# Kernel tuning notes

Measured on AMD Instinct MI355X. Metric: run time of the kernel, lower is better.

Reference implementation:

```python
import jax, jax.numpy as jnp
import numpy as np

B = 1024
NUM_DENSE = 13
NUM_SPARSE = 26
VOCAB = 100000
EMB_DIM = 16
BOT = [512, 256, 64, 16]
TOP = [1024, 512, 256]
D_INT = BOT[-1] + NUM_SPARSE * EMB_DIM  # 432
OUT_INT = D_INT * (D_INT + 1) // 2      # 93528


def setup_inputs() -> dict:
    key = jax.random.key(0)
    ks = jax.random.split(key, 32)
    inp = {
        "dense_features": jax.random.normal(ks[0], (B, NUM_DENSE), jnp.float32),
        "sparse_features": jax.random.randint(ks[1], (B, NUM_SPARSE), 0, VOCAB),
        "emb_tables": jax.random.normal(ks[2], (NUM_SPARSE, VOCAB, EMB_DIM), jnp.float32) * 0.02,
    }
    # bottom MLP weights (in, out) convention
    dims = [NUM_DENSE] + BOT
    for i in range(len(BOT)):
        inp[f"bw{i}"] = jax.random.normal(ks[3 + i], (dims[i], dims[i + 1]), jnp.float32) * 0.02
        inp[f"bb{i}"] = jnp.zeros((dims[i + 1],), jnp.float32)
    tdims = [BOT[-1] + OUT_INT] + TOP + [1]
    for i in range(len(TOP) + 1):
        inp[f"tw{i}"] = jax.random.normal(ks[10 + i], (tdims[i], tdims[i + 1]), jnp.float32) * 0.02
        inp[f"tb{i}"] = jnp.zeros((tdims[i + 1],), jnp.float32)
    return inp


def _forward(dense_features, emb_tables, bws, bbs, tws, tbs, sparse_features):
    # bottom MLP: Linear+ReLU stacks
    h = dense_features
    for w, b in zip(bws, bbs):
        h = jax.nn.relu(h @ w + b)
    dense_out = h  # (B, 16)
    # embedding lookups: table t indexed by column t of sparse_features
    # emb_tables: (F, V, E); gather per-table then flatten -> (B, F*E)
    emb = jnp.take_along_axis(
        emb_tables[None],  # (1, F, V, E)
        sparse_features.T[None, :, :, None].transpose(0, 1, 2, 3) * 0 + sparse_features.T[None, :, :, None],
        axis=2,
    )  # placeholder avoided below
    # cleaner: vmap over tables
    emb = jax.vmap(lambda tbl, idx: tbl[idx], in_axes=(0, 1))(emb_tables, sparse_features)  # (F, B, E)
    emb = jnp.transpose(emb, (1, 0, 2)).reshape(dense_features.shape[0], -1)  # (B, F*E)
    x = jnp.concatenate([dense_out, emb], axis=1)  # (B, D_INT)
    # pairwise interaction: upper triangle (incl. diagonal) of outer product.
    iu0, iu1 = np.triu_indices(x.shape[1])
    inter = x[:, iu0] * x[:, iu1]  # (B, OUT_INT) -- only needed entries
    z = jnp.concatenate([dense_out, inter], axis=1)
    n_top = len(tws)
    for i, (w, b) in enumerate(zip(tws, tbs)):
        z = z @ w + b
        if i < n_top - 1:
            z = jax.nn.relu(z)
    return z


def reference(dense_features, sparse_features, emb_tables,
              bw0, bb0, bw1, bb1, bw2, bb2, bw3, bb3,
              tw0, tb0, tw1, tb1, tw2, tb2, tw3, tb3):
    bws = [bw0, bw1, bw2, bw3]
    bbs = [bb0, bb1, bb2, bb3]
    tws = [tw0, tw1, tw2, tw3]
    tbs = [tb0, tb1, tb2, tb3]
    return _forward(dense_features, emb_tables, bws, bbs, tws, tbs, sparse_features)
```

## Files before the change

### kernel.cpp

```cpp
#include <hip/hip_runtime.h>
#include <stdint.h>

typedef unsigned short ushort_t;
typedef __attribute__((ext_vector_type(4))) float f32x4;
typedef __attribute__((ext_vector_type(8))) short s16x8;

#define DEVFN static __device__ __forceinline__

constexpr int B_   = 1024;
constexpr int P_   = 93528;
constexpr int K1   = 93544;
constexpr int Kp   = 94208;
constexpr int SPLITS = 16;
constexpr int KCH  = Kp / SPLITS;
constexpr int KSTEPS = KCH / 64;

DEVFN ushort_t f2bf(float f) {
  union { float f; unsigned int u; } x; x.f = f;
  unsigned int r = x.u + 0x7FFFu + ((x.u >> 16) & 1u);
  return (ushort_t)(r >> 16);
}

DEVFN void gload_lds16(const void* g, void* l) {
  __builtin_amdgcn_global_load_lds((const __attribute__((address_space(1))) unsigned int*)g,
                                   (__attribute__((address_space(3))) unsigned int*)l, 16, 0, 0);
}

__global__ __launch_bounds__(256) void k_iu(int* __restrict__ iu, float* __restrict__ xT) {
  int k = blockIdx.x * 256 + threadIdx.x;
  if (blockIdx.x < 8) {
    int idx = blockIdx.x * 256 + threadIdx.x;
    xT[432 * 1024 + idx] = (idx < 1024) ? 1.f : 0.f;
  }
  if (k >= Kp) return;
  int v;
  if (k < 16) v = k | (432 << 16);
  else if (k >= K1) v = 433 | (433 << 16);
  else {
    int p = k - 16;
    float s = sqrtf((float)(748225 - 8 * p));
    int i = (int)((865.0f - s) * 0.5f);
    if (i < 0) i = 0; if (i > 431) i = 431;
    while (i < 431 && (i + 1) * (865 - (i + 1)) / 2 <= p) ++i;
    while (i > 0 && i * (865 - i) / 2 > p) --i;
    int j = i + (p - i * (865 - i) / 2);
    v = i | (j << 16);
  }
  iu[k] = v;
}

__global__ __launch_bounds__(256) void k_bot(const float* __restrict__ dense,
    const float* __restrict__ bw0, const float* __restrict__ bb0,
    const float* __restrict__ bw1, const float* __restrict__ bb1,
    const float* __restrict__ bw2, const float* __restrict__ bb2,
    const float* __restrict__ bw3, const float* __restrict__ bb3,
    float* __restrict__ xT) {
  __shared__ float xs[16 * 13];
  __shared__ float h1[16 * 512];
  __shared__ float h2[16 * 256];
  __shared__ float h3[16 * 64];
  int t = threadIdx.x, m0 = blockIdx.x * 16;
  if (t < 208) xs[t] = dense[m0 * 13 + t];
  __syncthreads();
  #pragma unroll
  for (int h = 0; h < 2; ++h) {
    int n = h * 256 + t;
    float a[16];
    float bv = bb0[n];
    #pragma unroll
    for (int r = 0; r < 16; ++r) a[r] = bv;
    for (int k = 0; k < 13; ++k) {
      float w = bw0[k * 512 + n];
      #pragma unroll
      for (int r = 0; r < 16; ++r) a[r] = fmaf(xs[r * 13 + k], w, a[r]);
    }
    #pragma unroll
    for (int r = 0; r < 16; ++r) h1[r * 512 + n] = fmaxf(a[r], 0.f);
  }
  __syncthreads();
  {
    int n = t;
    float a[16];
    float bv = bb1[n];
    #pragma unroll
    for (int r = 0; r < 16; ++r) a[r] = bv;
    for (int k = 0; k < 512; ++k) {
      float w = bw1[k * 256 + n];
      #pragma unroll
      for (int r = 0; r < 16; ++r) a[r] = fmaf(h1[r * 512 + k], w, a[r]);
    }
    #pragma unroll
    for (int r = 0; r < 16; ++r) h2[r * 256 + n] = fmaxf(a[r], 0.f);
  }
  __syncthreads();
  {
    int n = t & 63, r0 = t >> 6;
    float a[4];
    float bv = bb2[n];
    #pragma unroll
    for (int i = 0; i < 4; ++i) a[i] = bv;
    for (int k = 0; k < 256; ++k) {
      float w = bw2[k * 64 + n];
      #pragma unroll
      for (int i = 0; i < 4; ++i) a[i] = fmaf(h2[(r0 + 4 * i) * 256 + k], w, a[i]);
    }
    #pragma unroll
    for (int i = 0; i < 4; ++i) h3[(r0 + 4 * i) * 64 + n] = fmaxf(a[i], 0.f);
  }
  __syncthreads();
  {
    int n = t & 15, r = t >> 4;
    float a = bb3[n];
    for (int k = 0; k < 64; ++k) a = fmaf(h3[r * 64 + k], bw3[k * 16 + n], a);
    xT[(size_t)n * B_ + m0 + r] = fmaxf(a, 0.f);
  }
}

template<int K, int N>
__global__ __launch_bounds__(256) void k_sgemm(const float* __restrict__ A,
                                               const float* __restrict__ W,
                                               const float* __restrict__ bias,
                                               float* __restrict__ C) {
  __shared__ float As[16][34];
  __shared__ float Bs[16][68];
  int t = threadIdx.x;
  int m0 = blockIdx.x * 32, n0 = blockIdx.y * 64;
  int tx = t & 15, ty = t >> 4;
  float acc[2][4];
  #pragma unroll
  for (int j = 0; j < 2; ++j)
    #pragma unroll
    for (int q = 0; q < 4; ++q) acc[j][q] = 0.f;
  int ar = t >> 3, ak = (t & 7) * 2;
  int bk = t >> 4, bn = (t & 15) * 4;
  for (int k0 = 0; k0 < K; k0 += 16) {
    float2 av = *(const float2*)&A[(size_t)(m0 + ar) * K + k0 + ak];
    float4 bv = *(const float4*)&W[(size_t)(k0 + bk) * N + n0 + bn];
    __syncthreads();
    As[ak][ar] = av.x; As[ak + 1][ar] = av.y;
    *(float4*)&Bs[bk][bn] = bv;
    __syncthreads();
    #pragma unroll
    for (int k = 0; k < 16; ++k) {
      float2 a = *(const float2*)&As[k][ty * 2];
      float4 b = *(const float4*)&Bs[k][tx * 4];
      acc[0][0] = fmaf(a.x, b.x, acc[0][0]); acc[0][1] = fmaf(a.x, b.y, acc[0][1]);
      acc[0][2] = fmaf(a.x, b.z, acc[0][2]); acc[0][3] = fmaf(a.x, b.w, acc[0][3]);
      acc[1][0] = fmaf(a.y, b.x, acc[1][0]); acc[1][1] = fmaf(a.y, b.y, acc[1][1]);
      acc[1][2] = fmaf(a.y, b.z, acc[1][2]); acc[1][3] = fmaf(a.y, b.w, acc[1][3]);
    }
  }
  #pragma unroll
  for (int j = 0; j < 2; ++j) {
    int m = m0 + ty * 2 + j;
    float4 o;
    o.x = fmaxf(acc[j][0] + bias[n0 + tx * 4 + 0], 0.f);
    o.y = fmaxf(acc[j][1] + bias[n0 + tx * 4 + 1], 0.f);
    o.z = fmaxf(acc[j][2] + bias[n0 + tx * 4 + 2], 0.f);
    o.w = fmaxf(acc[j][3] + bias[n0 + tx * 4 + 3], 0.f);
    *(float4*)&C[(size_t)m * N + n0 + tx * 4] = o;
  }
}

__global__ __launch_bounds__(256) void k_emb(const int* __restrict__ sparse,
                                             const float* __restrict__ tbl,
                                             float* __restrict__ xT) {
  int f = blockIdx.x;
  int b = blockIdx.y * 256 + threadIdx.x;
  int idx = sparse[(size_t)b * 26 + f];
  const float4* src = (const float4*)(tbl + ((size_t)f * 100000 + idx) * 16);
  #pragma unroll
  for (int q = 0; q < 4; ++q) {
    float4 v = src[q];
    int r = 16 + f * 16 + q * 4;
    xT[(size_t)(r + 0) * B_ + b] = v.x;
    xT[(size_t)(r + 1) * B_ + b] = v.y;
    xT[(size_t)(r + 2) * B_ + b] = v.z;
    xT[(size_t)(r + 3) * B_ + b] = v.w;
  }
}

__global__ __launch_bounds__(256, 4) void k_genz(const float* __restrict__ xT,
                                                 const int* __restrict__ iu,
                                                 ushort_t* __restrict__ Z) {
  __shared__ int ls_iu[512];
  int t = threadIdx.x, l = t & 63, w = t >> 6;
  int mb = blockIdx.x * 64;
  int kt = blockIdx.y * 512;
  ls_iu[t] = iu[kt + t];
  ls_iu[256 + t] = iu[kt + 256 + t];
  __syncthreads();
  uint32_t moff = mb + l;
  int kw = w * 128;
  #pragma unroll 2
  for (int g = 0; g < 16; ++g) {
    int kloc = kw + g * 8;
    int4 ij0 = *(const int4*)&ls_iu[kloc];
    int4 ij1 = *(const int4*)&ls_iu[kloc + 4];
    float p[8];
    {
      int v0 = ij0.x, v1 = ij0.y, v2 = ij0.z, v3 = ij0.w;
      p[0] = xT[(uint32_t)((v0 & 0xFFFF) << 10) + moff] * xT[(uint32_t)((v0 >> 16) << 10) + moff];
      p[1] = xT[(uint32_t)((v1 & 0xFFFF) << 10) + moff] * xT[(uint32_t)((v1 >> 16) << 10) + moff];
      p[2] = xT[(uint32_t)((v2 & 0xFFFF) << 10) + moff] * xT[(uint32_t)((v2 >> 16) << 10) + moff];
      p[3] = xT[(uint32_t)((v3 & 0xFFFF) << 10) + moff] * xT[(uint32_t)((v3 >> 16) << 10) + moff];
      v0 = ij1.x; v1 = ij1.y; v2 = ij1.z; v3 = ij1.w;
      p[4] = xT[(uint32_t)((v0 & 0xFFFF) << 10) + moff] * xT[(uint32_t)((v0 >> 16) << 10) + moff];
      p[5] = xT[(uint32_t)((v1 & 0xFFFF) << 10) + moff] * xT[(uint32_t)((v1 >> 16) << 10) + moff];
      p[6] = xT[(uint32_t)((v2 & 0xFFFF) << 10) + moff] * xT[(uint32_t)((v2 >> 16) << 10) + moff];
      p[7] = xT[(uint32_t)((v3 & 0xFFFF) << 10) + moff] * xT[(uint32_t)((v3 >> 16) << 10) + moff];
    }
    union { uint32_t w[4]; int4 v4; } o;
    asm("v_cvt_pk_bf16_f32 %0, %1, %2" : "=v"(o.w[0]) : "v"(p[0]), "v"(p[1]));
    asm("v_cvt_pk_bf16_f32 %0, %1, %2" : "=v"(o.w[1]) : "v"(p[2]), "v"(p[3]));
    asm("v_cvt_pk_bf16_f32 %0, %1, %2" : "=v"(o.w[2]) : "v"(p[4]), "v"(p[5]));
    asm("v_cvt_pk_bf16_f32 %0, %1, %2" : "=v"(o.w[3]) : "v"(p[6]), "v"(p[7]));
    int kglob = kt + kloc;
    *(int4*)&Z[((size_t)(kglob >> 3) * 1024 + moff) * 8] = o.v4;
  }
}

__global__ __launch_bounds__(256) void k_wt(const float* __restrict__ tw0,
                                            ushort_t* __restrict__ WT) {
  __shared__ ushort_t ls[256 * 68];
  int t = threadIdx.x;
  int k0 = blockIdx.x * 256, n0 = blockIdx.y * 64;
  int kr = t >> 2, c4 = t & 3;
  #pragma unroll
  for (int pass = 0; pass < 4; ++pass) {
    int kl = pass * 64 + kr;
    int k = k0 + kl;
    #pragma unroll
    for (int q = 0; q < 4; ++q) {
      float4 v = make_float4(0.f, 0.f, 0.f, 0.f);
      if (k < K1) v = *(const float4*)&tw0[(size_t)k * 1024 + n0 + q * 16 + c4 * 4];
      ushort_t* d = &ls[kl * 68 + q * 16 + c4 * 4];
      d[0] = f2bf(v.x); d[1] = f2bf(v.y); d[2] = f2bf(v.z); d[3] = f2bf(v.w);
    }
  }
  __syncthreads();
  int nl = t >> 2, kq = t & 3;
  ushort_t* dst = WT + (size_t)(n0 + nl) * Kp + k0 + kq * 64;
  #pragma unroll
  for (int j = 0; j < 8; ++j) {
    union { ushort_t u[8]; int4 v; } o;
    #pragma unroll
    for (int e = 0; e < 8; ++e) o.u[e] = ls[(kq * 64 + j * 8 + e) * 68 + nl];
    *(int4*)(dst + j * 8) = o.v;
  }
}

__global__ __launch_bounds__(512, 2) void k_gemm(const ushort_t* __restrict__ Z,
                                                 const ushort_t* __restrict__ WT,
                                                 float* __restrict__ part) {
  __shared__ ushort_t lds[65536];
  int t = threadIdx.x;
  int bid = blockIdx.x;
  int s = bid >> 4, tile = bid & 15;
  int m0 = (tile >> 2) * 256, n0 = (tile & 3) * 256;
  int kb = s * KCH;

  int rr = t >> 3, cc = t & 7;
  int cs = cc ^ (rr & 7);
  const ushort_t* pa0 = Z + (((size_t)(kb >> 3) + cs) * 1024 + m0 + rr) * 8;
  const ushort_t* pb0 = WT + (size_t)(n0 + rr) * Kp + kb + cs * 8;
  const size_t rowStrideB = (size_t)64 * Kp;
  int l0 = t * 8;

  int w = t >> 6, l = t & 63;
  int wm = (w >> 2) * 128, wn = (w & 3) * 64;
  int lhi = l >> 4, llo = l & 15;

  f32x4 acc[8][4];
  #pragma unroll
  for (int a = 0; a < 8; ++a)
    #pragma unroll
    for (int b = 0; b < 4; ++b) acc[a][b] = f32x4{0.f, 0.f, 0.f, 0.f};

  #pragma unroll
  for (int i = 0; i < 4; ++i)
    gload_lds16(pb0 + i * rowStrideB, &lds[32768 + i * 4096 + l0]);
  gload_lds16(pa0,            &lds[0 * 4096 + l0]);
  gload_lds16(pa0 + 2 * 512,  &lds[2 * 4096 + l0]);
  gload_lds16(pa0 + 1 * 512,  &lds[1 * 4096 + l0]);
  gload_lds16(pa0 + 3 * 512,  &lds[3 * 4096 + l0]);

  for (int tt = 0; tt < KSTEPS; ++tt) {
    const ushort_t* Ab = &lds[(tt & 1) * 16384];
    const ushort_t* Bb = &lds[32768 + (tt & 1) * 16384];
    bool pf = (tt + 1 < KSTEPS);
    ushort_t* dA = &lds[((tt + 1) & 1) * 16384];
    ushort_t* dB = &lds[32768 + ((tt + 1) & 1) * 16384];
    const ushort_t* sA = pa0 + (size_t)(tt + 1) * 65536;
    const ushort_t* sB = pb0 + (size_t)(tt + 1) * 64;
    s16x8 bf[4][2];

    asm volatile("s_waitcnt vmcnt(2)" ::: "memory");
    __builtin_amdgcn_s_barrier();
    __builtin_amdgcn_sched_barrier(0);
    if (pf) {
      gload_lds16(sB,              dB + l0);
      gload_lds16(sB + rowStrideB, dB + 4096 + l0);
    }
    #pragma unroll
    for (int nf = 0; nf < 4; ++nf)
      #pragma unroll
      for (int ks = 0; ks < 2; ++ks) {
        int row = wn + nf * 16 + llo;
        int ch = (ks * 4 + lhi) ^ (row & 7);
        bf[nf][ks] = *(const s16x8*)&Bb[row * 64 + ch * 8];
      }
    #pragma unroll
    for (int q = 0; q < 4; ++q) {
      if (q == 1 && pf) {
        gload_lds16(sB + 2 * rowStrideB, dB + 2 * 4096 + l0);
        gload_lds16(sB + 3 * rowStrideB, dB + 3 * 4096 + l0);
      }
      if (q == 2) {
        if (pf) asm volatile("s_waitcnt vmcnt(4)" ::: "memory");
        else    asm volatile("s_waitcnt vmcnt(0)" ::: "memory");
        __builtin_amdgcn_s_barrier();
        __builtin_amdgcn_sched_barrier(0);
        if (pf) {
          gload_lds16(sA,           dA + l0);
          gload_lds16(sA + 2 * 512, dA + 2 * 4096 + l0);
        }
      }
      if (q == 3 && pf) {
        gload_lds16(sA + 1 * 512, dA + 1 * 4096 + l0);
        gload_lds16(sA + 3 * 512, dA + 3 * 4096 + l0);
      }
      s16x8 af[2][2];
      #pragma unroll
      for (int j = 0; j < 2; ++j)
        #pragma unroll
        for (int ks = 0; ks < 2; ++ks) {
          int row = wm + (q * 2 + j) * 16 + llo;
          int ch = (ks * 4 + lhi) ^ (row & 7);
          af[j][ks] = *(const s16x8*)&Ab[row * 64 + ch * 8];
        }
      __builtin_amdgcn_s_setprio(1);
      #pragma unroll
      for (int j = 0; j < 2; ++j)
        #pragma unroll
        for (int nf = 0; nf < 4; ++nf)
          #pragma unroll
          for (int ks = 0; ks < 2; ++ks)
            acc[q * 2 + j][nf] = __builtin_amdgcn_mfma_f32_16x16x32_bf16(af[j][ks], bf[nf][ks], acc[q * 2 + j][nf], 0, 0, 0);
      __builtin_amdgcn_s_setprio(0);
    }
  }

  float* pbase = part + ((size_t)s << 20);
  #pragma unroll
  for (int mf = 0; mf < 8; ++mf)
    #pragma unroll
    for (int nf = 0; nf < 4; ++nf) {
      int n = n0 + wn + nf * 16 + llo;
      #pragma unroll
      for (int r = 0; r < 4; ++r) {
        int m = m0 + wm + mf * 16 + lhi * 4 + r;
        pbase[(size_t)m * 1024 + n] = acc[mf][nf][r];
      }
    }
}

__global__ __launch_bounds__(256) void k_red(const float* __restrict__ part,
                                             const float* __restrict__ bias,
                                             float* __restrict__ z1) {
  int idx = blockIdx.x * 256 + threadIdx.x;
  float a = bias[idx & 1023];
  #pragma unroll
  for (int s = 0; s < SPLITS; ++s) a += part[((size_t)s << 20) + idx];
  z1[idx] = fmaxf(a, 0.f);
}

__global__ __launch_bounds__(256) void k_last(const float* __restrict__ z3,
                                              const float* __restrict__ w,
                                              const float* __restrict__ bias,
                                              float* __restrict__ out) {
  int t = threadIdx.x, l = t & 63, wv = t >> 6;
  int m = blockIdx.x * 4 + wv;
  float s = 0.f;
  #pragma unroll
  for (int c = 0; c < 4; ++c) s = fmaf(z3[(size_t)m * 256 + c * 64 + l], w[c * 64 + l], s);
  #pragma unroll
  for (int off = 32; off; off >>= 1) s += __shfl_down(s, off, 64);
  if (l == 0) out[m] = s + bias[0];
}

__global__ __launch_bounds__(256) void k_z1init(const float* __restrict__ bias, float* __restrict__ z1) {
  int idx = blockIdx.x * 256 + threadIdx.x;
  z1[idx] = bias[idx & 1023];
}
__global__ __launch_bounds__(256) void k_relu(float* __restrict__ z1) {
  int idx = blockIdx.x * 256 + threadIdx.x;
  z1[idx] = fmaxf(z1[idx], 0.f);
}
constexpr int FB_S = 8;
__global__ __launch_bounds__(256) void k_fbgemm(const float* __restrict__ xT,
                                                const int* __restrict__ iu,
                                                const float* __restrict__ tw0,
                                                float* __restrict__ z1) {
  __shared__ float zs[32 * 64];
  __shared__ float wsb[32 * 64];
  int t = threadIdx.x;
  int m0 = blockIdx.x * 64, n0 = blockIdx.y * 64, s = blockIdx.z;
  int kch = (K1 + FB_S - 1) / FB_S;
  int k0 = s * kch, kend = min(k0 + kch, K1);
  float acc[16];
  #pragma unroll
  for (int q = 0; q < 16; ++q) acc[q] = 0.f;
  int mm = t & 63, ng = t >> 6;
  for (int kk = k0; kk < kend; kk += 32) {
    __syncthreads();
    for (int sl = t; sl < 2048; sl += 256) {
      int kloc = sl >> 6, v6 = sl & 63;
      int k = kk + kloc;
      float zv = 0.f, wv = 0.f;
      if (k < kend) {
        int ij = iu[k];
        int i = ij & 0xFFFF, j = ij >> 16;
        zv = xT[(size_t)i * B_ + m0 + v6] * xT[(size_t)j * B_ + m0 + v6];
        wv = tw0[(size_t)k * 1024 + n0 + v6];
      }
      zs[kloc * 64 + v6] = zv;
      wsb[kloc * 64 + v6] = wv;
    }
    __syncthreads();
    #pragma unroll 4
    for (int kloc = 0; kloc < 32; ++kloc) {
      float zv = zs[kloc * 64 + mm];
      #pragma unroll
      for (int q = 0; q < 16; ++q)
        acc[q] = fmaf(zv, wsb[kloc * 64 + ng * 16 + q], acc[q]);
    }
  }
  #pragma unroll
  for (int q = 0; q < 16; ++q)
    atomicAdd(&z1[(size_t)(m0 + mm) * 1024 + n0 + ng * 16 + q], acc[q]);
}

extern "C" void kernel_launch(void* const* d_in, const int* in_sizes, int n_in,
                              void* d_out, int out_size, void* d_ws, size_t ws_size,
                              hipStream_t stream) {
  const float* dense  = (const float*)d_in[0];
  const int*   sparse = (const int*)  d_in[1];
  const float* emb    = (const float*)d_in[2];
  const float* bw0 = (const float*)d_in[3];  const float* bb0 = (const float*)d_in[4];
  const float* bw1 = (const float*)d_in[5];  const float* bb1 = (const float*)d_in[6];
  const float* bw2 = (const float*)d_in[7];  const float* bb2 = (const float*)d_in[8];
  const float* bw3 = (const float*)d_in[9];  const float* bb3 = (const float*)d_in[10];
  const float* tw0 = (const float*)d_in[11]; const float* tb0 = (const float*)d_in[12];
  const float* tw1 = (const float*)d_in[13]; const float* tb1 = (const float*)d_in[14];
  const float* tw2 = (const float*)d_in[15]; const float* tb2 = (const float*)d_in[16];
  const float* tw3 = (const float*)d_in[17]; const float* tb3 = (const float*)d_in[18];
  float* out = (float*)d_out;

  char* ws = (char*)d_ws;
  size_t off = 0;
  auto alloc = [&](size_t bytes) -> char* {
    char* p = ws + off;
    off = (off + bytes + 255) & ~(size_t)255;
    return p;
  };
  float* xT = (float*)alloc((size_t)434 * 1024 * 4);
  int*   iu = (int*)  alloc((size_t)Kp * 4);
  float* z1 = (float*)alloc((size_t)1024 * 1024 * 4);
  float* z2 = (float*)alloc((size_t)1024 * 512 * 4);
  float* z3 = (float*)alloc((size_t)1024 * 256 * 4);
  ushort_t* Z    = (ushort_t*)alloc((size_t)1024 * Kp * 2);
  ushort_t* WT   = (ushort_t*)alloc((size_t)1024 * Kp * 2);
  float*    part = (float*)   alloc((size_t)SPLITS * 1024 * 1024 * 4);
  bool big = (off <= ws_size);

  k_iu<<<368, 256, 0, stream>>>(iu, xT);
  k_bot<<<64, 256, 0, stream>>>(dense, bw0, bb0, bw1, bb1, bw2, bb2, bw3, bb3, xT);
  k_emb<<<dim3(26, 4), 256, 0, stream>>>(sparse, emb, xT);

  if (big) {
    k_genz<<<dim3(16, 184), 256, 0, stream>>>(xT, iu, Z);
    k_wt<<<dim3(368, 16), 256, 0, stream>>>(tw0, WT);
    k_gemm<<<256, 512, 0, stream>>>(Z, WT, part);
    k_red<<<4096, 256, 0, stream>>>(part, tb0, z1);
  } else {
    k_z1init<<<4096, 256, 0, stream>>>(tb0, z1);
    k_fbgemm<<<dim3(16, 16, FB_S), 256, 0, stream>>>(xT, iu, tw0, z1);
    k_relu<<<4096, 256, 0, stream>>>(z1);
  }

  k_sgemm<1024, 512><<<dim3(32, 8), 256, 0, stream>>>(z1, tw1, tb1, z2);
  k_sgemm<512, 256><<<dim3(32, 4), 256, 0, stream>>>(z2, tw2, tb2, z3);
  k_last<<<256, 256, 0, stream>>>(z3, tw3, tb3, out);
}
```

Before: 581.8 us.

## Merge preprocessing kernels, interleave Z/WT generation, and restructure GEMM prefetch schedule

Folds the index-table, bottom-MLP and embedding kernels into one launch using block-range dispatch. The Z-generation and weight-transpose kernels are merged into one launch that interleaves their blocks, so the two memory-bound jobs share the GPU. The main GEMM now prefetches B two steps ahead and A one step ahead, with adjusted waitcnt values and extra sched_barriers. This cuts launch overhead and is meant to hide load latency better, at the cost of more complex and fragile vmcnt accounting.

```diff
diff --git a/kernel.cpp b/kernel.cpp
--- a/kernel.cpp
+++ b/kernel.cpp
@@ -26,94 +26,317 @@
                                    (__attribute__((address_space(3))) unsigned int*)l, 16, 0, 0);
 }
 
-__global__ __launch_bounds__(256) void k_iu(int* __restrict__ iu, float* __restrict__ xT) {
-  int k = blockIdx.x * 256 + threadIdx.x;
-  if (blockIdx.x < 8) {
-    int idx = blockIdx.x * 256 + threadIdx.x;
-    xT[432 * 1024 + idx] = (idx < 1024) ? 1.f : 0.f;
-  }
-  if (k >= Kp) return;
-  int v;
-  if (k < 16) v = k | (432 << 16);
-  else if (k >= K1) v = 433 | (433 << 16);
-  else {
-    int p = k - 16;
-    float s = sqrtf((float)(748225 - 8 * p));
-    int i = (int)((865.0f - s) * 0.5f);
-    if (i < 0) i = 0; if (i > 431) i = 431;
-    while (i < 431 && (i + 1) * (865 - (i + 1)) / 2 <= p) ++i;
-    while (i > 0 && i * (865 - i) / 2 > p) --i;
-    int j = i + (p - i * (865 - i) / 2);
-    v = i | (j << 16);
-  }
-  iu[k] = v;
-}
-
-__global__ __launch_bounds__(256) void k_bot(const float* __restrict__ dense,
+__global__ __launch_bounds__(256) void k_pre(const float* __restrict__ dense,
+    const int* __restrict__ sparse, const float* __restrict__ tbl,
     const float* __restrict__ bw0, const float* __restrict__ bb0,
     const float* __restrict__ bw1, const float* __restrict__ bb1,
     const float* __restrict__ bw2, const float* __restrict__ bb2,
     const float* __restrict__ bw3, const float* __restrict__ bb3,
-    float* __restrict__ xT) {
-  __shared__ float xs[16 * 13];
-  __shared__ float h1[16 * 512];
-  __shared__ float h2[16 * 256];
-  __shared__ float h3[16 * 64];
-  int t = threadIdx.x, m0 = blockIdx.x * 16;
-  if (t < 208) xs[t] = dense[m0 * 13 + t];
-  __syncthreads();
-  #pragma unroll
-  for (int h = 0; h < 2; ++h) {
-    int n = h * 256 + t;
-    float a[16];
-    float bv = bb0[n];
-    #pragma unroll
-    for (int r = 0; r < 16; ++r) a[r] = bv;
-    for (int k = 0; k < 13; ++k) {
-      float w = bw0[k * 512 + n];
-      #pragma unroll
-      for (int r = 0; r < 16; ++r) a[r] = fmaf(xs[r * 13 + k], w, a[r]);
-    }
-    #pragma unroll
-    for (int r = 0; r < 16; ++r) h1[r * 512 + n] = fmaxf(a[r], 0.f);
-  }
-  __syncthreads();
-  {
-    int n = t;
-    float a[16];
-    float bv = bb1[n];
-    #pragma unroll
-    for (int r = 0; r < 16; ++r) a[r] = bv;
-    for (int k = 0; k < 512; ++k) {
-      float w = bw1[k * 256 + n];
-      #pragma unroll
-      for (int r = 0; r < 16; ++r) a[r] = fmaf(h1[r * 512 + k], w, a[r]);
-    }
-    #pragma unroll
-    for (int r = 0; r < 16; ++r) h2[r * 256 + n] = fmaxf(a[r], 0.f);
-  }
-  __syncthreads();
-  {
-    int n = t & 63, r0 = t >> 6;
-    float a[4];
-    float bv = bb2[n];
-    #pragma unroll
-    for (int i = 0; i < 4; ++i) a[i] = bv;
-    for (int k = 0; k < 256; ++k) {
-      float w = bw2[k * 64 + n];
-      #pragma unroll
-      for (int i = 0; i < 4; ++i) a[i] = fmaf(h2[(r0 + 4 * i) * 256 + k], w, a[i]);
-    }
-    #pragma unroll
-    for (int i = 0; i < 4; ++i) h3[(r0 + 4 * i) * 64 + n] = fmaxf(a[i], 0.f);
-  }
-  __syncthreads();
-  {
-    int n = t & 15, r = t >> 4;
-    float a = bb3[n];
-    for (int k = 0; k < 64; ++k) a = fmaf(h3[r * 64 + k], bw3[k * 16 + n], a);
-    xT[(size_t)n * B_ + m0 + r] = fmaxf(a, 0.f);
-  }
+    int* __restrict__ iu, float* __restrict__ xT) {
+  __shared__ float sm[13520];
+  int bid = blockIdx.x, t = threadIdx.x;
+  if (bid < 368) {
+    int k = bid * 256 + t;
+    if (bid < 8) {
+      int idx = bid * 256 + t;
+      xT[432 * 1024 + idx] = (idx < 1024) ? 1.f : 0.f;
+    }
+    if (k >= Kp) return;
+    int v;
+    if (k < 16) v = k | (432 << 16);
+    else if (k >= K1) v = 433 | (433 << 16);
+    else {
+      int p = k - 16;
+      float s = sqrtf((float)(748225 - 8 * p));
+      int i = (int)((865.0f - s) * 0.5f);
+      if (i < 0) i = 0; if (i > 431) i = 431;
+      while (i < 431 && (i + 1) * (865 - (i + 1)) / 2 <= p) ++i;
+      while (i > 0 && i * (865 - i) / 2 > p) --i;
+      int j = i + (p - i * (865 - i) / 2);
+      v = i | (j << 16);
+    }
+    iu[k] = v;
+  } else if (bid < 432) {
+    float* xs = sm;
+    float* h1 = sm + 208;
+    float* h2 = h1 + 8192;
+    float* h3 = h2 + 4096;
+    int m0 = (bid - 368) * 16;
+    if (t < 208) xs[t] = dense[m0 * 13 + t];
+    __syncthreads();
+    #pragma unroll
+    for (int h = 0; h < 2; ++h) {
+      int n = h * 256 + t;
+      float a[16];
+      float bv = bb0[n];
+      #pragma unroll
+      for (int r = 0; r < 16; ++r) a[r] = bv;
+      for (int k = 0; k < 13; ++k) {
+        float w = bw0[k * 512 + n];
+        #pragma unroll
+        for (int r = 0; r < 16; ++r) a[r] = fmaf(xs[r * 13 + k], w, a[r]);
+      }
+      #pragma unroll
+      for (int r = 0; r < 16; ++r) h1[r * 512 + n] = fmaxf(a[r], 0.f);
+    }
+    __syncthreads();
+    {
+      int n = t;
+      float a[16];
+      float bv = bb1[n];
+      #pragma unroll
+      for (int r = 0; r < 16; ++r) a[r] = bv;
+      for (int k = 0; k < 512; ++k) {
+        float w = bw1[k * 256 + n];
+        #pragma unroll
+        for (int r = 0; r < 16; ++r) a[r] = fmaf(h1[r * 512 + k], w, a[r]);
+      }
+      #pragma unroll
+      for (int r = 0; r < 16; ++r) h2[r * 256 + n] = fmaxf(a[r], 0.f);
+    }
+    __syncthreads();
+    {
+      int n = t & 63, r0 = t >> 6;
+      float a[4];
+      float bv = bb2[n];
+      #pragma unroll
+      for (int i = 0; i < 4; ++i) a[i] = bv;
+      for (int k = 0; k < 256; ++k) {
+        float w = bw2[k * 64 + n];
+        #pragma unroll
+        for (int i = 0; i < 4; ++i) a[i] = fmaf(h2[(r0 + 4 * i) * 256 + k], w, a[i]);
+      }
+      #pragma unroll
+      for (int i = 0; i < 4; ++i) h3[(r0 + 4 * i) * 64 + n] = fmaxf(a[i], 0.f);
+    }
+    __syncthreads();
+    {
+      int n = t & 15, r = t >> 4;
+      float a = bb3[n];
+      for (int k = 0; k < 64; ++k) a = fmaf(h3[r * 64 + k], bw3[k * 16 + n], a);
+      xT[(size_t)n * B_ + m0 + r] = fmaxf(a, 0.f);
+    }
+  } else {
+    int e = bid - 432;
+    int f = e >> 2;
+    int b = (e & 3) * 256 + t;
+    int idx = sparse[(size_t)b * 26 + f];
+    const float4* src = (const float4*)(tbl + ((size_t)f * 100000 + idx) * 16);
+    #pragma unroll
+    for (int q = 0; q < 4; ++q) {
+      float4 v = src[q];
+      int r = 16 + f * 16 + q * 4;
+      xT[(size_t)(r + 0) * B_ + b] = v.x;
+      xT[(size_t)(r + 1) * B_ + b] = v.y;
+      xT[(size_t)(r + 2) * B_ + b] = v.z;
+      xT[(size_t)(r + 3) * B_ + b] = v.w;
+    }
+  }
+}
+
+__global__ __launch_bounds__(256, 4) void k_gz(const float* __restrict__ xT,
+                                               const int* __restrict__ iu,
+                                               const float* __restrict__ tw0,
+                                               ushort_t* __restrict__ Z,
+                                               ushort_t* __restrict__ WT) {
+  __shared__ char smem[256 * 68 * 2];
+  int bid = blockIdx.x, t = threadIdx.x;
+  int r3 = bid % 3;
+  if (r3 == 0) {
+    int idx = bid / 3;
+    int* ls_iu = (int*)smem;
+    int l = t & 63, w = t >> 6;
+    int mb = (idx & 15) * 64;
+    int kt = (idx >> 4) * 512;
+    ls_iu[t] = iu[kt + t];
+    ls_iu[256 + t] = iu[kt + 256 + t];
+    __syncthreads();
+    uint32_t moff = mb + l;
+    int kw = w * 128;
+    #pragma unroll 2
+    for (int g = 0; g < 16; ++g) {
+      int kloc = kw + g * 8;
+      int4 ij0 = *(const int4*)&ls_iu[kloc];
+      int4 ij1 = *(const int4*)&ls_iu[kloc + 4];
+      float p[8];
+      {
+        int v0 = ij0.x, v1 = ij0.y, v2 = ij0.z, v3 = ij0.w;
+        p[0] = xT[(uint32_t)((v0 & 0xFFFF) << 10) + moff] * xT[(uint32_t)((v0 >> 16) << 10) + moff];
+        p[1] = xT[(uint32_t)((v1 & 0xFFFF) << 10) + moff] * xT[(uint32_t)((v1 >> 16) << 10) + moff];
+        p[2] = xT[(uint32_t)((v2 & 0xFFFF) << 10) + moff] * xT[(uint32_t)((v2 >> 16) << 10) + moff];
+        p[3] = xT[(uint32_t)((v3 & 0xFFFF) << 10) + moff] * xT[(uint32_t)((v3 >> 16) << 10) + moff];
+        v0 = ij1.x; v1 = ij1.y; v2 = ij1.z; v3 = ij1.w;
+        p[4] = xT[(uint32_t)((v0 & 0xFFFF) << 10) + moff] * xT[(uint32_t)((v0 >> 16) << 10) + moff];
+        p[5] = xT[(uint32_t)((v1 & 0xFFFF) << 10) + moff] * xT[(uint32_t)((v1 >> 16) << 10) + moff];
+        p[6] = xT[(uint32_t)((v2 & 0xFFFF) << 10) + moff] * xT[(uint32_t)((v2 >> 16) << 10) + moff];
+        p[7] = xT[(uint32_t)((v3 & 0xFFFF) << 10) + moff] * xT[(uint32_t)((v3 >> 16) << 10) + moff];
+      }
+      union { uint32_t w4[4]; int4 v4; } o;
+      asm("v_cvt_pk_bf16_f32 %0, %1, %2" : "=v"(o.w4[0]) : "v"(p[0]), "v"(p[1]));
+      asm("v_cvt_pk_bf16_f32 %0, %1, %2" : "=v"(o.w4[1]) : "v"(p[2]), "v"(p[3]));
+      asm("v_cvt_pk_bf16_f32 %0, %1, %2" : "=v"(o.w4[2]) : "v"(p[4]), "v"(p[5]));
+      asm("v_cvt_pk_bf16_f32 %0, %1, %2" : "=v"(o.w4[3]) : "v"(p[6]), "v"(p[7]));
+      int kglob = kt + kloc;
+      *(int4*)&Z[((size_t)(kglob >> 3) * 1024 + moff) * 8] = o.v4;
+    }
+  } else {
+    int idx = (bid / 3) * 2 + r3 - 1;
+    ushort_t* ls = (ushort_t*)smem;
+    int k0 = (idx % 368) * 256, n0 = (idx / 368) * 64;
+    int kr = t >> 2, c4 = t & 3;
+    #pragma unroll
+    for (int pass = 0; pass < 4; ++pass) {
+      int kl = pass * 64 + kr;
+      int k = k0 + kl;
+      #pragma unroll
+      for (int q = 0; q < 4; ++q) {
+        float4 v = make_float4(0.f, 0.f, 0.f, 0.f);
+        if (k < K1) v = *(const float4*)&tw0[(size_t)k * 1024 + n0 + q * 16 + c4 * 4];
+        ushort_t* d = &ls[kl * 68 + q * 16 + c4 * 4];
+        d[0] = f2bf(v.x); d[1] = f2bf(v.y); d[2] = f2bf(v.z); d[3] = f2bf(v.w);
+      }
+    }
+    __syncthreads();
+    int nl = t >> 2, kq = t & 3;
+    ushort_t* dst = WT + (size_t)(n0 + nl) * Kp + k0 + kq * 64;
+    #pragma unroll
+    for (int j = 0; j < 8; ++j) {
+      union { ushort_t u[8]; int4 v; } o;
+      #pragma unroll
+      for (int e = 0; e < 8; ++e) o.u[e] = ls[(kq * 64 + j * 8 + e) * 68 + nl];
+      *(int4*)(dst + j * 8) = o.v;
+    }
+  }
+}
+
+__global__ __launch_bounds__(512, 2) void k_gemm(const ushort_t* __restrict__ Z,
+                                                 const ushort_t* __restrict__ WT,
+                                                 float* __restrict__ part) {
+  __shared__ ushort_t lds[65536];
+  int t = threadIdx.x;
+  int bid = blockIdx.x;
+  int s = bid >> 4, tile = bid & 15;
+  int m0 = (tile >> 2) * 256, n0 = (tile & 3) * 256;
+  int kb = s * KCH;
+
+  int rr = t >> 3, cc = t & 7;
+  int cs = cc ^ (rr & 7);
+  const ushort_t* pa0 = Z + (((size_t)(kb >> 3) + cs) * 1024 + m0 + rr) * 8;
+  const ushort_t* pb0 = WT + (size_t)(n0 + rr) * Kp + kb + cs * 8;
+  const size_t rowStrideB = (size_t)64 * Kp;
+  int l0 = t * 8;
+
+  int w = t >> 6, l = t & 63;
+  int wm = (w >> 2) * 128, wn = (w & 3) * 64;
+  int lhi = l >> 4, llo = l & 15;
+
+  f32x4 acc[8][4];
+  #pragma unroll
+  for (int a = 0; a < 8; ++a)
+    #pragma unroll
+    for (int b = 0; b < 4; ++b) acc[a][b] = f32x4{0.f, 0.f, 0.f, 0.f};
+
+  #pragma unroll
+  for (int i = 0; i < 4; ++i)
+    gload_lds16(pb0 + i * rowStrideB, &lds[32768 + i * 4096 + l0]);
+  gload_lds16(pa0,           &lds[0 * 4096 + l0]);
+  gload_lds16(pa0 + 2 * 512, &lds[2 * 4096 + l0]);
+  gload_lds16(pa0 + 1 * 512, &lds[1 * 4096 + l0]);
+  gload_lds16(pa0 + 3 * 512, &lds[3 * 4096 + l0]);
+  #pragma unroll
+  for (int i = 0; i < 4; ++i)
+    gload_lds16(pb0 + 64 + i * rowStrideB, &lds[32768 + 16384 + i * 4096 + l0]);
+
+  for (int tt = 0; tt < KSTEPS; ++tt) {
+    const ushort_t* Ab = &lds[(tt & 1) * 16384];
+    const ushort_t* Bb = &lds[32768 + (tt & 1) * 16384];
+    bool pf  = (tt + 1 < KSTEPS);
+    bool pf2 = (tt + 2 < KSTEPS);
+    ushort_t* dA  = &lds[((tt + 1) & 1) * 16384];
+    ushort_t* dB2 = &lds[32768 + (tt & 1) * 16384];
+    const ushort_t* sA  = pa0 + (size_t)(tt + 1) * 65536;
+    const ushort_t* sB2 = pb0 + (size_t)(tt + 2) * 64;
+    s16x8 bf[4][2];
+
+    if (pf) asm volatile("s_waitcnt vmcnt(6)" ::: "memory");
+    else    asm volatile("s_waitcnt vmcnt(2)" ::: "memory");
+    __builtin_amdgcn_s_barrier();
+    __builtin_amdgcn_sched_barrier(0);
+    if (pf) {
+      gload_lds16(sA,           dA + l0);
+      gload_lds16(sA + 2 * 512, dA + 2 * 4096 + l0);
+    }
+    #pragma unroll
+    for (int nf = 0; nf < 4; ++nf)
+      #pragma unroll
+      for (int ks = 0; ks < 2; ++ks) {
+        int row = wn + nf * 16 + llo;
+        int ch = (ks * 4 + lhi) ^ (row & 7);
+        bf[nf][ks] = *(const s16x8*)&Bb[row * 64 + ch * 8];
+      }
+    #pragma unroll
+    for (int q = 0; q < 4; ++q) {
+      if (q == 1 && pf) {
+        gload_lds16(sA + 1 * 512, dA + 1 * 4096 + l0);
+        gload_lds16(sA + 3 * 512, dA + 3 * 4096 + l0);
+      }
+      if (q == 2) {
+        if (pf) asm volatile("s_waitcnt vmcnt(8)" ::: "memory");
+        else    asm volatile("s_waitcnt vmcnt(0)" ::: "memory");
+        __builtin_amdgcn_s_barrier();
+        __builtin_amdgcn_sched_barrier(0);
+        if (pf2) {
+          #pragma unroll
+          for (int i = 0; i < 4; ++i)
+            gload_lds16(sB2 + i * rowStrideB, dB2 + i * 4096 + l0);
+        }
+      }
+      s16x8 af[2][2];
+      #pragma unroll
+      for (int j = 0; j < 2; ++j)
+        #pragma unroll
+        for (int ks = 0; ks < 2; ++ks) {
+          int row = wm + (q * 2 + j) * 16 + llo;
+          int ch = (ks * 4 + lhi) ^ (row & 7);
+          af[j][ks] = *(const s16x8*)&Ab[row * 64 + ch * 8];
+        }
+      asm volatile("s_waitcnt lgkmcnt(0)" ::: "memory");
+      __builtin_amdgcn_sched_barrier(0);
+      __builtin_amdgcn_s_setprio(1);
+      #pragma unroll
+      for (int j = 0; j < 2; ++j)
+        #pragma unroll
+        for (int nf = 0; nf < 4; ++nf)
+          #pragma unroll
+          for (int ks = 0; ks < 2; ++ks)
+            acc[q * 2 + j][nf] = __builtin_amdgcn_mfma_f32_16x16x32_bf16(af[j][ks], bf[nf][ks], acc[q * 2 + j][nf], 0, 0, 0);
+      __builtin_amdgcn_s_setprio(0);
+      __builtin_amdgcn_sched_barrier(0);
+    }
+  }
+
+  float* pbase = part + ((size_t)s << 20);
+  #pragma unroll
+  for (int mf = 0; mf < 8; ++mf)
+    #pragma unroll
+    for (int nf = 0; nf < 4; ++nf) {
+      int n = n0 + wn + nf * 16 + llo;
+      #pragma unroll
+      for (int r = 0; r < 4; ++r) {
+        int m = m0 + wm + mf * 16 + lhi * 4 + r;
+        pbase[(size_t)m * 1024 + n] = acc[mf][nf][r];
+      }
+    }
+}
+
+__global__ __launch_bounds__(256) void k_red(const float* __restrict__ part,
+                                             const float* __restrict__ bias,
+                                             float* __restrict__ z1) {
+  int idx = blockIdx.x * 256 + threadIdx.x;
+  float a = bias[idx & 1023];
+  #pragma unroll
+  for (int s = 0; s < SPLITS; ++s) a += part[((size_t)s << 20) + idx];
+  z1[idx] = fmaxf(a, 0.f);
 }
 
 template<int K, int N>
@@ -160,219 +383,6 @@
     o.w = fmaxf(acc[j][3] + bias[n0 + tx * 4 + 3], 0.f);
     *(float4*)&C[(size_t)m * N + n0 + tx * 4] = o;
   }
-}
-
-__global__ __launch_bounds__(256) void k_emb(const int* __restrict__ sparse,
-                                             const float* __restrict__ tbl,
-                                             float* __restrict__ xT) {
-  int f = blockIdx.x;
-  int b = blockIdx.y * 256 + threadIdx.x;
-  int idx = sparse[(size_t)b * 26 + f];
-  const float4* src = (const float4*)(tbl + ((size_t)f * 100000 + idx) * 16);
-  #pragma unroll
-  for (int q = 0; q < 4; ++q) {
-    float4 v = src[q];
-    int r = 16 + f * 16 + q * 4;
-    xT[(size_t)(r + 0) * B_ + b] = v.x;
-    xT[(size_t)(r + 1) * B_ + b] = v.y;
-    xT[(size_t)(r + 2) * B_ + b] = v.z;
-    xT[(size_t)(r + 3) * B_ + b] = v.w;
-  }
-}
-
-__global__ __launch_bounds__(256, 4) void k_genz(const float* __restrict__ xT,
-                                                 const int* __restrict__ iu,
-                                                 ushort_t* __restrict__ Z) {
-  __shared__ int ls_iu[512];
-  int t = threadIdx.x, l = t & 63, w = t >> 6;
-  int mb = blockIdx.x * 64;
-  int kt = blockIdx.y * 512;
-  ls_iu[t] = iu[kt + t];
-  ls_iu[256 + t] = iu[kt + 256 + t];
-  __syncthreads();
-  uint32_t moff = mb + l;
-  int kw = w * 128;
-  #pragma unroll 2
-  for (int g = 0; g < 16; ++g) {
-    int kloc = kw + g * 8;
-    int4 ij0 = *(const int4*)&ls_iu[kloc];
-    int4 ij1 = *(const int4*)&ls_iu[kloc + 4];
-    float p[8];
-    {
-      int v0 = ij0.x, v1 = ij0.y, v2 = ij0.z, v3 = ij0.w;
-      p[0] = xT[(uint32_t)((v0 & 0xFFFF) << 10) + moff] * xT[(uint32_t)((v0 >> 16) << 10) + moff];
-      p[1] = xT[(uint32_t)((v1 & 0xFFFF) << 10) + moff] * xT[(uint32_t)((v1 >> 16) << 10) + moff];
-      p[2] = xT[(uint32_t)((v2 & 0xFFFF) << 10) + moff] * xT[(uint32_t)((v2 >> 16) << 10) + moff];
-      p[3] = xT[(uint32_t)((v3 & 0xFFFF) << 10) + moff] * xT[(uint32_t)((v3 >> 16) << 10) + moff];
-      v0 = ij1.x; v1 = ij1.y; v2 = ij1.z; v3 = ij1.w;
-      p[4] = xT[(uint32_t)((v0 & 0xFFFF) << 10) + moff] * xT[(uint32_t)((v0 >> 16) << 10) + moff];
-      p[5] = xT[(uint32_t)((v1 & 0xFFFF) << 10) + moff] * xT[(uint32_t)((v1 >> 16) << 10) + moff];
-      p[6] = xT[(uint32_t)((v2 & 0xFFFF) << 10) + moff] * xT[(uint32_t)((v2 >> 16) << 10) + moff];
-      p[7] = xT[(uint32_t)((v3 & 0xFFFF) << 10) + moff] * xT[(uint32_t)((v3 >> 16) << 10) + moff];
-    }
-    union { uint32_t w[4]; int4 v4; } o;
-    asm("v_cvt_pk_bf16_f32 %0, %1, %2" : "=v"(o.w[0]) : "v"(p[0]), "v"(p[1]));
-    asm("v_cvt_pk_bf16_f32 %0, %1, %2" : "=v"(o.w[1]) : "v"(p[2]), "v"(p[3]));
-    asm("v_cvt_pk_bf16_f32 %0, %1, %2" : "=v"(o.w[2]) : "v"(p[4]), "v"(p[5]));
-    asm("v_cvt_pk_bf16_f32 %0, %1, %2" : "=v"(o.w[3]) : "v"(p[6]), "v"(p[7]));
-    int kglob = kt + kloc;
-    *(int4*)&Z[((size_t)(kglob >> 3) * 1024 + moff) * 8] = o.v4;
-  }
-}
-
-__global__ __launch_bounds__(256) void k_wt(const float* __restrict__ tw0,
-                                            ushort_t* __restrict__ WT) {
-  __shared__ ushort_t ls[256 * 68];
-  int t = threadIdx.x;
-  int k0 = blockIdx.x * 256, n0 = blockIdx.y * 64;
-  int kr = t >> 2, c4 = t & 3;
-  #pragma unroll
-  for (int pass = 0; pass < 4; ++pass) {
-    int kl = pass * 64 + kr;
-    int k = k0 + kl;
-    #pragma unroll
-    for (int q = 0; q < 4; ++q) {
-      float4 v = make_float4(0.f, 0.f, 0.f, 0.f);
-      if (k < K1) v = *(const float4*)&tw0[(size_t)k * 1024 + n0 + q * 16 + c4 * 4];
-      ushort_t* d = &ls[kl * 68 + q * 16 + c4 * 4];
-      d[0] = f2bf(v.x); d[1] = f2bf(v.y); d[2] = f2bf(v.z); d[3] = f2bf(v.w);
-    }
-  }
-  __syncthreads();
-  int nl = t >> 2, kq = t & 3;
-  ushort_t* dst = WT + (size_t)(n0 + nl) * Kp + k0 + kq * 64;
-  #pragma unroll
-  for (int j = 0; j < 8; ++j) {
-    union { ushort_t u[8]; int4 v; } o;
-    #pragma unroll
-    for (int e = 0; e < 8; ++e) o.u[e] = ls[(kq * 64 + j * 8 + e) * 68 + nl];
-    *(int4*)(dst + j * 8) = o.v;
-  }
-}
-
-__global__ __launch_bounds__(512, 2) void k_gemm(const ushort_t* __restrict__ Z,
-                                                 const ushort_t* __restrict__ WT,
-                                                 float* __restrict__ part) {
-  __shared__ ushort_t lds[65536];
-  int t = threadIdx.x;
-  int bid = blockIdx.x;
-  int s = bid >> 4, tile = bid & 15;
-  int m0 = (tile >> 2) * 256, n0 = (tile & 3) * 256;
-  int kb = s * KCH;
-
-  int rr = t >> 3, cc = t & 7;
-  int cs = cc ^ (rr & 7);
-  const ushort_t* pa0 = Z + (((size_t)(kb >> 3) + cs) * 1024 + m0 + rr) * 8;
-  const ushort_t* pb0 = WT + (size_t)(n0 + rr) * Kp + kb + cs * 8;
-  const size_t rowStrideB = (size_t)64 * Kp;
-  int l0 = t * 8;
-
-  int w = t >> 6, l = t & 63;
-  int wm = (w >> 2) * 128, wn = (w & 3) * 64;
-  int lhi = l >> 4, llo = l & 15;
-
-  f32x4 acc[8][4];
-  #pragma unroll
-  for (int a = 0; a < 8; ++a)
-    #pragma unroll
-    for (int b = 0; b < 4; ++b) acc[a][b] = f32x4{0.f, 0.f, 0.f, 0.f};
-
-  #pragma unroll
-  for (int i = 0; i < 4; ++i)
-    gload_lds16(pb0 + i * rowStrideB, &lds[32768 + i * 4096 + l0]);
-  gload_lds16(pa0,            &lds[0 * 4096 + l0]);
-  gload_lds16(pa0 + 2 * 512,  &lds[2 * 4096 + l0]);
-  gload_lds16(pa0 + 1 * 512,  &lds[1 * 4096 + l0]);
-  gload_lds16(pa0 + 3 * 512,  &lds[3 * 4096 + l0]);
-
-  for (int tt = 0; tt < KSTEPS; ++tt) {
-    const ushort_t* Ab = &lds[(tt & 1) * 16384];
-    const ushort_t* Bb = &lds[32768 + (tt & 1) * 16384];
-    bool pf = (tt + 1 < KSTEPS);
-    ushort_t* dA = &lds[((tt + 1) & 1) * 16384];
-    ushort_t* dB = &lds[32768 + ((tt + 1) & 1) * 16384];
-    const ushort_t* sA = pa0 + (size_t)(tt + 1) * 65536;
-    const ushort_t* sB = pb0 + (size_t)(tt + 1) * 64;
-    s16x8 bf[4][2];
-
-    asm volatile("s_waitcnt vmcnt(2)" ::: "memory");
-    __builtin_amdgcn_s_barrier();
-    __builtin_amdgcn_sched_barrier(0);
-    if (pf) {
-      gload_lds16(sB,              dB + l0);
-      gload_lds16(sB + rowStrideB, dB + 4096 + l0);
-    }
-    #pragma unroll
-    for (int nf = 0; nf < 4; ++nf)
-      #pragma unroll
-      for (int ks = 0; ks < 2; ++ks) {
-        int row = wn + nf * 16 + llo;
-        int ch = (ks * 4 + lhi) ^ (row & 7);
-        bf[nf][ks] = *(const s16x8*)&Bb[row * 64 + ch * 8];
-      }
-    #pragma unroll
-    for (int q = 0; q < 4; ++q) {
-      if (q == 1 && pf) {
-        gload_lds16(sB + 2 * rowStrideB, dB + 2 * 4096 + l0);
-        gload_lds16(sB + 3 * rowStrideB, dB + 3 * 4096 + l0);
-      }
-      if (q == 2) {
-        if (pf) asm volatile("s_waitcnt vmcnt(4)" ::: "memory");
-        else    asm volatile("s_waitcnt vmcnt(0)" ::: "memory");
-        __builtin_amdgcn_s_barrier();
-        __builtin_amdgcn_sched_barrier(0);
-        if (pf) {
-          gload_lds16(sA,           dA + l0);
-          gload_lds16(sA + 2 * 512, dA + 2 * 4096 + l0);
-        }
-      }
-      if (q == 3 && pf) {
-        gload_lds16(sA + 1 * 512, dA + 1 * 4096 + l0);
-        gload_lds16(sA + 3 * 512, dA + 3 * 4096 + l0);
-      }
-      s16x8 af[2][2];
-      #pragma unroll
-      for (int j = 0; j < 2; ++j)
-        #pragma unroll
-        for (int ks = 0; ks < 2; ++ks) {
-          int row = wm + (q * 2 + j) * 16 + llo;
-          int ch = (ks * 4 + lhi) ^ (row & 7);
-          af[j][ks] = *(const s16x8*)&Ab[row * 64 + ch * 8];
-        }
-      __builtin_amdgcn_s_setprio(1);
-      #pragma unroll
-      for (int j = 0; j < 2; ++j)
-        #pragma unroll
-        for (int nf = 0; nf < 4; ++nf)
-          #pragma unroll
-          for (int ks = 0; ks < 2; ++ks)
-            acc[q * 2 + j][nf] = __builtin_amdgcn_mfma_f32_16x16x32_bf16(af[j][ks], bf[nf][ks], acc[q * 2 + j][nf], 0, 0, 0);
-      __builtin_amdgcn_s_setprio(0);
-    }
-  }
-
-  float* pbase = part + ((size_t)s << 20);
-  #pragma unroll
-  for (int mf = 0; mf < 8; ++mf)
-    #pragma unroll
-    for (int nf = 0; nf < 4; ++nf) {
-      int n = n0 + wn + nf * 16 + llo;
-      #pragma unroll
-      for (int r = 0; r < 4; ++r) {
-        int m = m0 + wm + mf * 16 + lhi * 4 + r;
-        pbase[(size_t)m * 1024 + n] = acc[mf][nf][r];
-      }
-    }
-}
-
-__global__ __launch_bounds__(256) void k_red(const float* __restrict__ part,
-                                             const float* __restrict__ bias,
-                                             float* __restrict__ z1) {
-  int idx = blockIdx.x * 256 + threadIdx.x;
-  float a = bias[idx & 1023];
-  #pragma unroll
-  for (int s = 0; s < SPLITS; ++s) a += part[((size_t)s << 20) + idx];
-  z1[idx] = fmaxf(a, 0.f);
 }
 
 __global__ __launch_bounds__(256) void k_last(const float* __restrict__ z3,
@@ -474,13 +484,10 @@
   float*    part = (float*)   alloc((size_t)SPLITS * 1024 * 1024 * 4);
   bool big = (off <= ws_size);
 
-  k_iu<<<368, 256, 0, stream>>>(iu, xT);
-  k_bot<<<64, 256, 0, stream>>>(dense, bw0, bb0, bw1, bb1, bw2, bb2, bw3, bb3, xT);
-  k_emb<<<dim3(26, 4), 256, 0, stream>>>(sparse, emb, xT);
+  k_pre<<<536, 256, 0, stream>>>(dense, sparse, emb, bw0, bb0, bw1, bb1, bw2, bb2, bw3, bb3, iu, xT);
 
   if (big) {
-    k_genz<<<dim3(16, 184), 256, 0, stream>>>(xT, iu, Z);
-    k_wt<<<dim3(368, 16), 256, 0, stream>>>(tw0, WT);
+    k_gz<<<8832, 256, 0, stream>>>(xT, iu, tw0, Z, WT);
     k_gemm<<<256, 512, 0, stream>>>(Z, WT, part);
     k_red<<<4096, 256, 0, stream>>>(part, tb0, z1);
   } else {
```

Result: faster. 540.6 us (-7.1%).
